# Kernel tuning notes

Measured on AMD Instinct MI355X. Metric: run time of the kernel, lower is better.

The kernel has to match this reference:

```python
import jax, jax.numpy as jnp
import numpy as np

B, S, D, H = 4, 2048, 1024, 16
HD = D // H
EPS = 1e-5
MASKED_BIAS = -10000.0

def setup_inputs() -> dict:
    key = jax.random.key(0)
    ks = jax.random.split(key, 12)
    sd = 0.02
    return {
        "hidden_states": jax.random.normal(ks[0], (B, S, D), jnp.float32),
        "Wq": jax.random.normal(ks[1], (D, D), jnp.float32) * sd,
        "bq": jnp.zeros((D,), jnp.float32),
        "Wk": jax.random.normal(ks[2], (D, D), jnp.float32) * sd,
        "bk": jnp.zeros((D,), jnp.float32),
        "Wv": jax.random.normal(ks[3], (D, D), jnp.float32) * sd,
        "bv": jnp.zeros((D,), jnp.float32),
        "Wp": jax.random.normal(ks[4], (D, D), jnp.float32) * sd,
        "bp": jnp.zeros((D,), jnp.float32),
        "ln_g": jnp.ones((D,), jnp.float32),
        "ln_b": jnp.zeros((D,), jnp.float32),
    }

def reference(hidden_states, Wq, bq, Wk, bk, Wv, bv, Wp, bp, ln_g, ln_b):
    x = hidden_states  # [B,S,D]
    # QKV projections (nn.Linear: x @ W^T + b; here W stored as [D,D], use x@W)
    q = x @ Wq + bq
    k = x @ Wk + bk
    v = x @ Wv + bv
    # split heads -> [B,H,S,HD]
    def split(t):
        return t.reshape(B, S, H, HD).transpose(0, 2, 1, 3)
    q, k, v = split(q), split(k), split(v)
    # scaled scores [B,H,S,S]
    scores = jnp.einsum("bhqd,bhkd->bhqk", q, k) / jnp.float32(np.sqrt(HD))
    causal = jnp.tril(jnp.ones((S, S), bool))
    scores = jnp.where(causal[None, None], scores, jnp.float32(MASKED_BIAS))
    attn = jax.nn.softmax(scores, axis=-1)
    out = jnp.einsum("bhqk,bhkd->bhqd", attn, v)
    # merge heads -> [B,S,D]
    out = out.transpose(0, 2, 1, 3).reshape(B, S, D)
    out = out @ Wp + bp
    # residual + layernorm
    y = out + x
    mu = jnp.mean(y, axis=-1, keepdims=True)
    var = jnp.var(y, axis=-1, keepdims=True)
    y = (y - mu) * jax.lax.rsqrt(var + EPS) * ln_g + ln_b
    return y
```

## Files before the change

kernel.cpp:

```cpp
#include <hip/hip_runtime.h>
#include <math.h>

#define B_  4
#define S_  2048
#define D_  1024
#define H_  16
#define HD_ 64
#define M_  (B_*S_)

typedef unsigned int  uint;
typedef unsigned short ushort;

typedef __attribute__((ext_vector_type(8))) short bf16x8;
typedef __attribute__((ext_vector_type(4))) float f32x4;

#if __has_builtin(__builtin_amdgcn_exp2f)
#define EXP2(x) __builtin_amdgcn_exp2f(x)
#else
#define EXP2(x) exp2f(x)
#endif

__device__ __forceinline__ ushort f2bf(float x) {
    uint u = __float_as_uint(x);
    u += 0x7FFFu + ((u >> 16) & 1u);
    return (ushort)(u >> 16);
}
__device__ __forceinline__ uint pack2bf(float a, float b) {
    uint ua = __float_as_uint(a); ua += 0x7FFFu + ((ua >> 16) & 1u);
    uint ub = __float_as_uint(b); ub += 0x7FFFu + ((ub >> 16) & 1u);
    return (ua >> 16) | (ub & 0xFFFF0000u);
}

__global__ __launch_bounds__(256) void prep(const float* __restrict__ x,
                                            ushort* __restrict__ xb,
                                            const float* __restrict__ Wq,
                                            const float* __restrict__ Wk,
                                            const float* __restrict__ Wv,
                                            const float* __restrict__ Wp,
                                            ushort* __restrict__ wtq,
                                            ushort* __restrict__ wtk,
                                            ushort* __restrict__ wtv,
                                            ushort* __restrict__ wtp) {
    __shared__ float t[32][33];
    const int tid = threadIdx.x;
    if (blockIdx.z == 0) {
        const int idx = blockIdx.x * 256 + tid;
        const float4* p = (const float4*)(x + (size_t)idx * 8);
        float4 a = p[0], b = p[1];
        uint4 o;
        o.x = pack2bf(a.x, a.y); o.y = pack2bf(a.z, a.w);
        o.z = pack2bf(b.x, b.y); o.w = pack2bf(b.z, b.w);
        ((uint4*)xb)[idx] = o;
    } else {
        const int w = blockIdx.x >> 10;
        const int sub = blockIdx.x & 1023;
        const float* W = (w == 0) ? Wq : (w == 1) ? Wk : (w == 2) ? Wv : Wp;
        ushort* Wt     = (w == 0) ? wtq : (w == 1) ? wtk : (w == 2) ? wtv : wtp;
        const int nb = (sub & 31) * 32, kb = (sub >> 5) * 32;
        #pragma unroll
        for (int l = 0; l < 4; ++l) {
            int idx = tid + l * 256;
            int r = idx >> 5, c = idx & 31;
            t[r][c] = W[(size_t)(kb + r) * D_ + nb + c];
        }
        __syncthreads();
        #pragma unroll
        for (int l = 0; l < 4; ++l) {
            int idx = tid + l * 256;
            int nr = idx >> 5, kc = idx & 31;
            Wt[(size_t)(nb + nr) * D_ + kb + kc] = f2bf(t[kc][nr]);
        }
    }
}

#define GM 128
#define GN 128
#define GK 32

__device__ __forceinline__ void gemm_core(const ushort* __restrict__ A,
                                          const ushort* __restrict__ Bt,
                                          f32x4 acc[4][4], int m0, int n0) {
    __shared__ __align__(16) ushort As[GM * GK];
    __shared__ __align__(16) ushort Bs[GN * GK];
    const int tid  = threadIdx.x;
    const int wave = tid >> 6, lane = tid & 63;
    const int wm = (wave >> 1) * 64, wn = (wave & 1) * 64;
    const int fr = lane & 15, fq = lane >> 4;

    #pragma unroll
    for (int i = 0; i < 4; ++i)
        #pragma unroll
        for (int j = 0; j < 4; ++j) acc[i][j] = (f32x4){0.f, 0.f, 0.f, 0.f};

    for (int k0 = 0; k0 < D_; k0 += GK) {
        #pragma unroll
        for (int it = 0; it < 2; ++it) {
            int ch = it * 256 + tid;
            int r = ch >> 2, p = ch & 3;
            const ushort* ga = A  + (size_t)(m0 + r) * D_ + k0 + p * 8;
            const ushort* gb = Bt + (size_t)(n0 + r) * D_ + k0 + p * 8;
            ushort* la = As + (size_t)(it * 256 + wave * 64) * 8;
            ushort* lb = Bs + (size_t)(it * 256 + wave * 64) * 8;
            __builtin_amdgcn_global_load_lds(
                (const __attribute__((address_space(1))) void*)ga,
                (__attribute__((address_space(3))) void*)la, 16, 0, 0);
            __builtin_amdgcn_global_load_lds(
                (const __attribute__((address_space(1))) void*)gb,
                (__attribute__((address_space(3))) void*)lb, 16, 0, 0);
        }
        __syncthreads();

        bf16x8 af[4], bfr[4];
        #pragma unroll
        for (int i = 0; i < 4; ++i)
            af[i] = *(const bf16x8*)&As[(wm + 16 * i + fr) * GK + fq * 8];
        #pragma unroll
        for (int j = 0; j < 4; ++j)
            bfr[j] = *(const bf16x8*)&Bs[(wn + 16 * j + fr) * GK + fq * 8];
        #pragma unroll
        for (int i = 0; i < 4; ++i)
            #pragma unroll
            for (int j = 0; j < 4; ++j)
                acc[i][j] = __builtin_amdgcn_mfma_f32_16x16x32_bf16(af[i], bfr[j], acc[i][j], 0, 0, 0);
        __syncthreads();
    }
}

__global__ __launch_bounds__(256) void gemm_qkvt(const ushort* __restrict__ xb,
                                                 const ushort* __restrict__ wtq,
                                                 const ushort* __restrict__ wtk,
                                                 const ushort* __restrict__ wtv,
                                                 const float* __restrict__ bq,
                                                 const float* __restrict__ bk,
                                                 const float* __restrict__ bv,
                                                 ushort* __restrict__ qb,
                                                 ushort* __restrict__ kb,
                                                 ushort* __restrict__ vtb) {
    const int z = blockIdx.z;
    const int lane = threadIdx.x & 63, wave = threadIdx.x >> 6;
    const int wm = (wave >> 1) * 64, wn = (wave & 1) * 64;
    const int cr = (lane >> 4) * 4, cc = lane & 15;
    f32x4 acc[4][4];

    if (z < 2) {
        const int m0 = blockIdx.x * GM, n0 = blockIdx.y * GN;
        gemm_core(xb, z ? wtk : wtq, acc, m0, n0);
        const float* bias = z ? bk : bq;
        ushort* C = z ? kb : qb;
        const float sc = z ? 1.0f : 0.18033688f;
        #pragma unroll
        for (int j = 0; j < 4; ++j) {
            const int col = n0 + wn + 16 * j + cc;
            const float bs = bias[col];
            const int h = col >> 6, hd = col & 63;
            #pragma unroll
            for (int i = 0; i < 4; ++i)
                #pragma unroll
                for (int r = 0; r < 4; ++r) {
                    const int row = m0 + wm + 16 * i + cr + r;
                    const int bb = row >> 11, s = row & 2047;
                    C[(((size_t)bb * H_ + h) * S_ + s) * HD_ + hd] = f2bf((acc[i][j][r] + bs) * sc);
                }
        }
    } else {
        const int m0 = blockIdx.y * GM, n0 = blockIdx.x * GN;
        gemm_core(wtv, xb, acc, m0, n0);
        #pragma unroll
        for (int i = 0; i < 4; ++i)
            #pragma unroll
            for (int r = 0; r < 4; ++r) {
                const int f = m0 + wm + 16 * i + cr + r;
                const float bs = bv[f];
                const int h = f >> 6, hd = f & 63;
                #pragma unroll
                for (int j = 0; j < 4; ++j) {
                    const int t = n0 + wn + 16 * j + cc;
                    const int bb = t >> 11, s = t & 2047;
                    vtb[(((size_t)bb * H_ + h) * HD_ + hd) * S_ + s] = f2bf(acc[i][j][r] + bs);
                }
            }
    }
}

__global__ __launch_bounds__(256) void gemm_p(const ushort* __restrict__ A,
                                              const ushort* __restrict__ Bt,
                                              const float* __restrict__ bias,
                                              float* __restrict__ C) {
    const int m0 = blockIdx.y * GM, n0 = blockIdx.x * GN;
    f32x4 acc[4][4];
    gemm_core(A, Bt, acc, m0, n0);

    const int lane = threadIdx.x & 63, wave = threadIdx.x >> 6;
    const int wm = (wave >> 1) * 64, wn = (wave & 1) * 64;
    const int cr = (lane >> 4) * 4, cc = lane & 15;
    #pragma unroll
    for (int j = 0; j < 4; ++j) {
        const int col = n0 + wn + 16 * j + cc;
        const float bs = bias[col];
        #pragma unroll
        for (int i = 0; i < 4; ++i)
            #pragma unroll
            for (int r = 0; r < 4; ++r)
                C[(size_t)(m0 + wm + 16 * i + cr + r) * D_ + col] = acc[i][j][r] + bs;
    }
}

#define PST 40

__global__ __launch_bounds__(256) void attn_mfma(const ushort* __restrict__ qb,
                                                 const ushort* __restrict__ kb,
                                                 const ushort* __restrict__ vtb,
                                                 ushort* __restrict__ ob) {
    __shared__ __align__(16) ushort Ks[2][128 * 64];
    __shared__ __align__(16) ushort Vs[2][64 * 128];
    __shared__ __align__(16) ushort Pp[4][32 * PST];

    const int tid = threadIdx.x, wave = tid >> 6, lane = tid & 63;
    const int fr = lane & 15, fq = lane >> 4;
    const int hb = blockIdx.x;
    const int p  = blockIdx.y;
    const int b = hb >> 4, h = hb & 15;
    const size_t bh = (size_t)b * H_ + h;
    const ushort* qbase = qb + bh * S_ * HD_;
    const ushort* kbase = kb + bh * S_ * HD_;
    const ushort* vbase = vtb + bh * HD_ * S_;
    ushort* PpW = Pp[wave];
    const int xrw = (fr & 7) << 4;

    int kg[4], vg[4];
    #pragma unroll
    for (int i = 0; i < 4; ++i) {
        const int o = (i * 256 + tid) * 16;
        int r = o >> 7, cS = o & 127;
        kg[i] = r * 128 + (cS ^ ((r & 7) << 4));
        r = o >> 8; cS = o & 255;
        vg[i] = r * (S_ * 2) + (cS ^ ((r & 7) << 4));
    }

    for (int phase = 0; phase < 2; ++phase) {
        const int chunk = phase ? p : (15 - p);
        const int q0 = chunk * 128;
        const int wq0 = q0 + wave * 32;
        const int nkt = chunk + 1;

        bf16x8 qf[2][2];
        #pragma unroll
        for (int nt = 0; nt < 2; ++nt)
            #pragma unroll
            for (int kk = 0; kk < 2; ++kk)
                qf[nt][kk] = *(const bf16x8*)&qbase[(size_t)(wq0 + nt * 16 + fr) * HD_ + kk * 32 + fq * 8];

        f32x4 ot[4][2];
        #pragma unroll
        for (int mt = 0; mt < 4; ++mt)
            #pragma unroll
            for (int nt = 0; nt < 2; ++nt) ot[mt][nt] = (f32x4){0.f, 0.f, 0.f, 0.f};
        float lp[2] = {0.f, 0.f};

        int cur = 0;
        #pragma unroll
        for (int i = 0; i < 4; ++i) {
            __builtin_amdgcn_global_load_lds(
                (const __attribute__((address_space(1))) void*)((const char*)kbase + kg[i]),
                (__attribute__((address_space(3))) void*)(&Ks[0][(i * 256 + wave * 64) * 8]), 16, 0, 0);
            __builtin_amdgcn_global_load_lds(
                (const __attribute__((address_space(1))) void*)((const char*)vbase + vg[i]),
                (__attribute__((address_space(3))) void*)(&Vs[0][(i * 256 + wave * 64) * 8]), 16, 0, 0);
        }
        __syncthreads();

        for (int kt = 0; kt < nkt; ++kt) {
            if (kt + 1 < nkt) {
                const int kn = (kt + 1) * 128;
                #pragma unroll
                for (int i = 0; i < 4; ++i) {
                    __builtin_amdgcn_global_load_lds(
                        (const __attribute__((address_space(1))) void*)((const char*)kbase + (size_t)kn * 128 + kg[i]),
                        (__attribute__((address_space(3))) void*)(&Ks[cur ^ 1][(i * 256 + wave * 64) * 8]), 16, 0, 0);
                    __builtin_amdgcn_global_load_lds(
                        (const __attribute__((address_space(1))) void*)((const char*)vbase + (size_t)kn * 2 + vg[i]),
                        (__attribute__((address_space(3))) void*)(&Vs[cur ^ 1][(i * 256 + wave * 64) * 8]), 16, 0, 0);
                }
            }
            const int k0 = kt * 128;
            const ushort* Kb = Ks[cur];
            const ushort* Vb = Vs[cur];
            const bool last = (kt == nkt - 1);

            #pragma unroll
            for (int g = 0; g < 4; ++g) {
                bf16x8 kf[2][2];
                #pragma unroll
                for (int mtL = 0; mtL < 2; ++mtL) {
                    const int mt = 2 * g + mtL;
                    kf[mtL][0] = *(const bf16x8*)((const char*)Kb + (mt * 16 + fr) * 128 + ((fq * 16) ^ xrw));
                    kf[mtL][1] = *(const bf16x8*)((const char*)Kb + (mt * 16 + fr) * 128 + ((64 + fq * 16) ^ xrw));
                }
                f32x4 st[2][2];
                #pragma unroll
                for (int mtL = 0; mtL < 2; ++mtL) {
                    const int mt = 2 * g + mtL;
                    #pragma unroll
                    for (int nt = 0; nt < 2; ++nt) {
                        f32x4 t = (f32x4){0.f, 0.f, 0.f, 0.f};
                        if (k0 + mt * 16 <= wq0 + nt * 16 + 15) {
                            t = __builtin_amdgcn_mfma_f32_16x16x32_bf16(kf[mtL][0], qf[nt][0], t, 0, 0, 0);
                            t = __builtin_amdgcn_mfma_f32_16x16x32_bf16(kf[mtL][1], qf[nt][1], t, 0, 0, 0);
                        }
                        st[mtL][nt] = t;
                    }
                }
                #pragma unroll
                for (int nt = 0; nt < 2; ++nt) {
                    const int qrow = wq0 + nt * 16 + fr;
                    #pragma unroll
                    for (int mtL = 0; mtL < 2; ++mtL) {
                        const int kb0 = k0 + (2 * g + mtL) * 16 + fq * 4;
                        float pr[4];
                        #pragma unroll
                        for (int r = 0; r < 4; ++r) {
                            const float e = EXP2(st[mtL][nt][r]);
                            pr[r] = (last && (kb0 + r > qrow)) ? 0.f : e;
                        }
                        lp[nt] += (pr[0] + pr[1]) + (pr[2] + pr[3]);
                        uint2 w;
                        w.x = pack2bf(pr[0], pr[1]);
                        w.y = pack2bf(pr[2], pr[3]);
                        *(uint2*)&PpW[(nt * 16 + fr) * PST + mtL * 16 + fq * 4] = w;
                    }
                }
                bf16x8 vf[4];
                #pragma unroll
                for (int mt = 0; mt < 4; ++mt)
                    vf[mt] = *(const bf16x8*)((const char*)Vb + (mt * 16 + fr) * 256 + ((g * 64 + fq * 16) ^ xrw));
                #pragma unroll
                for (int nt = 0; nt < 2; ++nt) {
                    if (k0 + g * 32 <= wq0 + nt * 16 + 15) {
                        bf16x8 pf = *(const bf16x8*)&PpW[(nt * 16 + fr) * PST + fq * 8];
                        #pragma unroll
                        for (int mt = 0; mt < 4; ++mt)
                            ot[mt][nt] = __builtin_amdgcn_mfma_f32_16x16x32_bf16(vf[mt], pf, ot[mt][nt], 0, 0, 0);
                    }
                }
            }
            __syncthreads();
            cur ^= 1;
        }

        #pragma unroll
        for (int nt = 0; nt < 2; ++nt) {
            float l = lp[nt];
            l += __shfl_xor(l, 16);
            l += __shfl_xor(l, 32);
            const float inv = 1.0f / l;
            const int row = wq0 + nt * 16 + fr;
            #pragma unroll
            for (int mt = 0; mt < 4; ++mt) {
                uint2 w;
                w.x = pack2bf(ot[mt][nt][0] * inv, ot[mt][nt][1] * inv);
                w.y = pack2bf(ot[mt][nt][2] * inv, ot[mt][nt][3] * inv);
                *(uint2*)&ob[((size_t)b * S_ + row) * D_ + h * HD_ + mt * 16 + fq * 4] = w;
            }
        }
    }
}

__global__ __launch_bounds__(256) void resln(float* __restrict__ out,
                                             const float* __restrict__ x,
                                             const float* __restrict__ g,
                                             const float* __restrict__ bb) {
    __shared__ float red[256];
    const int row = blockIdx.x, tid = threadIdx.x;
    const size_t off = (size_t)row * D_ + tid * 4;

    float4 p  = *(const float4*)&out[off];
    float4 xr = *(const float4*)&x[off];
    float4 y  = make_float4(p.x + xr.x, p.y + xr.y, p.z + xr.z, p.w + xr.w);

    float sum = y.x + y.y + y.z + y.w;
    red[tid] = sum;
    __syncthreads();
    #pragma unroll
    for (int st = 128; st > 0; st >>= 1) {
        if (tid < st) red[tid] += red[tid + st];
        __syncthreads();
    }
    const float mu = red[0] * (1.0f / D_);
    __syncthreads();

    float dx = y.x - mu, dy = y.y - mu, dz = y.z - mu, dw = y.w - mu;
    red[tid] = dx * dx + dy * dy + dz * dz + dw * dw;
    __syncthreads();
    #pragma unroll
    for (int st = 128; st > 0; st >>= 1) {
        if (tid < st) red[tid] += red[tid + st];
        __syncthreads();
    }
    const float var = red[0] * (1.0f / D_);
    const float inv = rsqrtf(var + 1e-5f);

    float4 gg = *(const float4*)&g[tid * 4];
    float4 bv = *(const float4*)&bb[tid * 4];
    float4 r;
    r.x = dx * inv * gg.x + bv.x;
    r.y = dy * inv * gg.y + bv.y;
    r.z = dz * inv * gg.z + bv.z;
    r.w = dw * inv * gg.w + bv.w;
    *(float4*)&out[off] = r;
}

extern "C" void kernel_launch(void* const* d_in, const int* in_sizes, int n_in,
                              void* d_out, int out_size, void* d_ws, size_t ws_size,
                              hipStream_t stream) {
    const float* x    = (const float*)d_in[0];
    const float* Wq   = (const float*)d_in[1];
    const float* bq   = (const float*)d_in[2];
    const float* Wk   = (const float*)d_in[3];
    const float* bk   = (const float*)d_in[4];
    const float* Wv   = (const float*)d_in[5];
    const float* bv   = (const float*)d_in[6];
    const float* Wp   = (const float*)d_in[7];
    const float* bp   = (const float*)d_in[8];
    const float* ln_g = (const float*)d_in[9];
    const float* ln_b = (const float*)d_in[10];

    float* out = (float*)d_out;

    char* ws = (char*)d_ws;
    ushort* qb  = (ushort*)ws;
    ushort* kb  = (ushort*)(ws + (size_t)16 * (1 << 20));
    ushort* vtb = (ushort*)(ws + (size_t)32 * (1 << 20));
    ushort* xb  = (ushort*)(ws + (size_t)48 * (1 << 20));
    ushort* ob  = (ushort*)(ws + (size_t)64 * (1 << 20));
    ushort* wtq = (ushort*)(ws + (size_t)80 * (1 << 20));
    ushort* wtk = (ushort*)(ws + (size_t)82 * (1 << 20));
    ushort* wtv = (ushort*)(ws + (size_t)84 * (1 << 20));
    ushort* wtp = (ushort*)(ws + (size_t)86 * (1 << 20));

    prep<<<dim3(4096, 1, 2), 256, 0, stream>>>(x, xb, Wq, Wk, Wv, Wp, wtq, wtk, wtv, wtp);

    gemm_qkvt<<<dim3(M_ / GM, D_ / GN, 3), 256, 0, stream>>>(
        xb, wtq, wtk, wtv, bq, bk, bv, qb, kb, vtb);

    attn_mfma<<<dim3(64, 8, 1), 256, 0, stream>>>(qb, kb, vtb, ob);

    gemm_p<<<dim3(D_ / GN, M_ / GM), 256, 0, stream>>>(ob, wtp, bp, out);
    resln<<<M_, 256, 0, stream>>>(out, x, ln_g, ln_b);
}
```

Measured before the change: 292.0 us.

## Peel causal tail tile, software-pipeline QK MFMAs, vectorize QKV epilogue stores

The attention loop now peels the last (diagonal) key tile so full tiles run without masking checks. In those tiles the QK^T MFMAs for the next group are issued before the exp and PV work of the current group, with s_setprio raised around MFMA bursts to overlap matrix and VALU work. The QKV GEMM swaps its MFMA operand order so each lane holds 4 contiguous output features (or tokens for V^T) and writes packed 8-byte stores instead of scalar bf16 stores. This adds register pressure from the double-buffered score fragments.

New measurement: 282.2 us. -3.4%, faster.

```diff
diff --git a/kernel.cpp b/kernel.cpp
--- a/kernel.cpp
+++ b/kernel.cpp
@@ -77,6 +77,7 @@
 #define GN 128
 #define GK 32
 
+template <bool SWAP>
 __device__ __forceinline__ void gemm_core(const ushort* __restrict__ A,
                                           const ushort* __restrict__ Bt,
                                           f32x4 acc[4][4], int m0, int n0) {
@@ -121,7 +122,9 @@
         for (int i = 0; i < 4; ++i)
             #pragma unroll
             for (int j = 0; j < 4; ++j)
-                acc[i][j] = __builtin_amdgcn_mfma_f32_16x16x32_bf16(af[i], bfr[j], acc[i][j], 0, 0, 0);
+                acc[i][j] = SWAP
+                    ? __builtin_amdgcn_mfma_f32_16x16x32_bf16(bfr[j], af[i], acc[i][j], 0, 0, 0)
+                    : __builtin_amdgcn_mfma_f32_16x16x32_bf16(af[i], bfr[j], acc[i][j], 0, 0, 0);
         __syncthreads();
     }
 }
@@ -139,46 +142,49 @@
     const int z = blockIdx.z;
     const int lane = threadIdx.x & 63, wave = threadIdx.x >> 6;
     const int wm = (wave >> 1) * 64, wn = (wave & 1) * 64;
-    const int cr = (lane >> 4) * 4, cc = lane & 15;
+    const int cc = lane & 15, fq = lane >> 4;
+    const int m0 = blockIdx.x * GM, n0 = blockIdx.y * GN;
     f32x4 acc[4][4];
 
     if (z < 2) {
-        const int m0 = blockIdx.x * GM, n0 = blockIdx.y * GN;
-        gemm_core(xb, z ? wtk : wtq, acc, m0, n0);
+        gemm_core<true>(xb, z ? wtk : wtq, acc, m0, n0);
         const float* bias = z ? bk : bq;
         ushort* C = z ? kb : qb;
         const float sc = z ? 1.0f : 0.18033688f;
         #pragma unroll
         for (int j = 0; j < 4; ++j) {
-            const int col = n0 + wn + 16 * j + cc;
-            const float bs = bias[col];
-            const int h = col >> 6, hd = col & 63;
-            #pragma unroll
-            for (int i = 0; i < 4; ++i)
-                #pragma unroll
-                for (int r = 0; r < 4; ++r) {
-                    const int row = m0 + wm + 16 * i + cr + r;
-                    const int bb = row >> 11, s = row & 2047;
-                    C[(((size_t)bb * H_ + h) * S_ + s) * HD_ + hd] = f2bf((acc[i][j][r] + bs) * sc);
-                }
+            const int f0 = n0 + wn + 16 * j + fq * 4;
+            const float4 bs4 = *(const float4*)&bias[f0];
+            const int h = f0 >> 6, hd = f0 & 63;
+            #pragma unroll
+            for (int i = 0; i < 4; ++i) {
+                const int token = m0 + wm + 16 * i + cc;
+                const int bb = token >> 11, s = token & 2047;
+                const float v0 = (acc[i][j][0] + bs4.x) * sc;
+                const float v1 = (acc[i][j][1] + bs4.y) * sc;
+                const float v2 = (acc[i][j][2] + bs4.z) * sc;
+                const float v3 = (acc[i][j][3] + bs4.w) * sc;
+                uint2 w; w.x = pack2bf(v0, v1); w.y = pack2bf(v2, v3);
+                *(uint2*)&C[(((size_t)bb * H_ + h) * S_ + s) * HD_ + hd] = w;
+            }
         }
     } else {
-        const int m0 = blockIdx.y * GM, n0 = blockIdx.x * GN;
-        gemm_core(wtv, xb, acc, m0, n0);
-        #pragma unroll
-        for (int i = 0; i < 4; ++i)
-            #pragma unroll
-            for (int r = 0; r < 4; ++r) {
-                const int f = m0 + wm + 16 * i + cr + r;
+        gemm_core<false>(xb, wtv, acc, m0, n0);
+        #pragma unroll
+        for (int i = 0; i < 4; ++i) {
+            const int t0 = m0 + wm + 16 * i + fq * 4;
+            const int bb = t0 >> 11, s = t0 & 2047;
+            #pragma unroll
+            for (int j = 0; j < 4; ++j) {
+                const int f = n0 + wn + 16 * j + cc;
                 const float bs = bv[f];
                 const int h = f >> 6, hd = f & 63;
-                #pragma unroll
-                for (int j = 0; j < 4; ++j) {
-                    const int t = n0 + wn + 16 * j + cc;
-                    const int bb = t >> 11, s = t & 2047;
-                    vtb[(((size_t)bb * H_ + h) * HD_ + hd) * S_ + s] = f2bf(acc[i][j][r] + bs);
-                }
+                uint2 w;
+                w.x = pack2bf(acc[i][j][0] + bs, acc[i][j][1] + bs);
+                w.y = pack2bf(acc[i][j][2] + bs, acc[i][j][3] + bs);
+                *(uint2*)&vtb[(((size_t)bb * H_ + h) * HD_ + hd) * S_ + s] = w;
             }
+        }
     }
 }
 
@@ -188,7 +194,7 @@
                                               float* __restrict__ C) {
     const int m0 = blockIdx.y * GM, n0 = blockIdx.x * GN;
     f32x4 acc[4][4];
-    gemm_core(A, Bt, acc, m0, n0);
+    gemm_core<false>(A, Bt, acc, m0, n0);
 
     const int lane = threadIdx.x & 63, wave = threadIdx.x >> 6;
     const int wm = (wave >> 1) * 64, wn = (wave & 1) * 64;
@@ -206,6 +212,18 @@
 }
 
 #define PST 40
+
+#define STAGE(kt_, buf_) do {                                                   \
+    const int kn_ = (kt_) * 128;                                                \
+    _Pragma("unroll")                                                           \
+    for (int i_ = 0; i_ < 4; ++i_) {                                            \
+        __builtin_amdgcn_global_load_lds(                                       \
+            (const __attribute__((address_space(1))) void*)((const char*)kbase + (size_t)kn_ * 128 + kg[i_]), \
+            (__attribute__((address_space(3))) void*)(&Ks[buf_][(i_ * 256 + wave * 64) * 8]), 16, 0, 0); \
+        __builtin_amdgcn_global_load_lds(                                       \
+            (const __attribute__((address_space(1))) void*)((const char*)vbase + (size_t)kn_ * 2 + vg[i_]), \
+            (__attribute__((address_space(3))) void*)(&Vs[buf_][(i_ * 256 + wave * 64) * 8]), 16, 0, 0); \
+    } } while (0)
 
 __global__ __launch_bounds__(256) void attn_mfma(const ushort* __restrict__ qb,
                                                  const ushort* __restrict__ kb,
@@ -258,34 +276,92 @@
         float lp[2] = {0.f, 0.f};
 
         int cur = 0;
-        #pragma unroll
-        for (int i = 0; i < 4; ++i) {
-            __builtin_amdgcn_global_load_lds(
-                (const __attribute__((address_space(1))) void*)((const char*)kbase + kg[i]),
-                (__attribute__((address_space(3))) void*)(&Ks[0][(i * 256 + wave * 64) * 8]), 16, 0, 0);
-            __builtin_amdgcn_global_load_lds(
-                (const __attribute__((address_space(1))) void*)((const char*)vbase + vg[i]),
-                (__attribute__((address_space(3))) void*)(&Vs[0][(i * 256 + wave * 64) * 8]), 16, 0, 0);
-        }
+        STAGE(0, 0);
         __syncthreads();
 
-        for (int kt = 0; kt < nkt; ++kt) {
-            if (kt + 1 < nkt) {
-                const int kn = (kt + 1) * 128;
-                #pragma unroll
-                for (int i = 0; i < 4; ++i) {
-                    __builtin_amdgcn_global_load_lds(
-                        (const __attribute__((address_space(1))) void*)((const char*)kbase + (size_t)kn * 128 + kg[i]),
-                        (__attribute__((address_space(3))) void*)(&Ks[cur ^ 1][(i * 256 + wave * 64) * 8]), 16, 0, 0);
-                    __builtin_amdgcn_global_load_lds(
-                        (const __attribute__((address_space(1))) void*)((const char*)vbase + (size_t)kn * 2 + vg[i]),
-                        (__attribute__((address_space(3))) void*)(&Vs[cur ^ 1][(i * 256 + wave * 64) * 8]), 16, 0, 0);
-                }
-            }
-            const int k0 = kt * 128;
+        for (int kt = 0; kt < nkt - 1; ++kt) {
+            STAGE(kt + 1, cur ^ 1);
             const ushort* Kb = Ks[cur];
             const ushort* Vb = Vs[cur];
-            const bool last = (kt == nkt - 1);
+
+            bf16x8 kf[2][2][2];
+            f32x4  st[2][2][2];
+
+            #pragma unroll
+            for (int mtL = 0; mtL < 2; ++mtL) {
+                kf[0][mtL][0] = *(const bf16x8*)((const char*)Kb + (mtL * 16 + fr) * 128 + ((fq * 16) ^ xrw));
+                kf[0][mtL][1] = *(const bf16x8*)((const char*)Kb + (mtL * 16 + fr) * 128 + ((64 + fq * 16) ^ xrw));
+            }
+            __builtin_amdgcn_s_setprio(1);
+            #pragma unroll
+            for (int mtL = 0; mtL < 2; ++mtL)
+                #pragma unroll
+                for (int nt = 0; nt < 2; ++nt) {
+                    f32x4 t = (f32x4){0.f, 0.f, 0.f, 0.f};
+                    t = __builtin_amdgcn_mfma_f32_16x16x32_bf16(kf[0][mtL][0], qf[nt][0], t, 0, 0, 0);
+                    t = __builtin_amdgcn_mfma_f32_16x16x32_bf16(kf[0][mtL][1], qf[nt][1], t, 0, 0, 0);
+                    st[0][mtL][nt] = t;
+                }
+            __builtin_amdgcn_s_setprio(0);
+
+            #pragma unroll
+            for (int g = 0; g < 4; ++g) {
+                const int pc = g & 1, pn = pc ^ 1;
+                if (g < 3) {
+                    const int mtb = 2 * (g + 1);
+                    #pragma unroll
+                    for (int mtL = 0; mtL < 2; ++mtL) {
+                        kf[pn][mtL][0] = *(const bf16x8*)((const char*)Kb + ((mtb + mtL) * 16 + fr) * 128 + ((fq * 16) ^ xrw));
+                        kf[pn][mtL][1] = *(const bf16x8*)((const char*)Kb + ((mtb + mtL) * 16 + fr) * 128 + ((64 + fq * 16) ^ xrw));
+                    }
+                    __builtin_amdgcn_s_setprio(1);
+                    #pragma unroll
+                    for (int mtL = 0; mtL < 2; ++mtL)
+                        #pragma unroll
+                        for (int nt = 0; nt < 2; ++nt) {
+                            f32x4 t = (f32x4){0.f, 0.f, 0.f, 0.f};
+                            t = __builtin_amdgcn_mfma_f32_16x16x32_bf16(kf[pn][mtL][0], qf[nt][0], t, 0, 0, 0);
+                            t = __builtin_amdgcn_mfma_f32_16x16x32_bf16(kf[pn][mtL][1], qf[nt][1], t, 0, 0, 0);
+                            st[pn][mtL][nt] = t;
+                        }
+                    __builtin_amdgcn_s_setprio(0);
+                }
+                #pragma unroll
+                for (int nt = 0; nt < 2; ++nt) {
+                    #pragma unroll
+                    for (int mtL = 0; mtL < 2; ++mtL) {
+                        float pr[4];
+                        #pragma unroll
+                        for (int r = 0; r < 4; ++r) pr[r] = EXP2(st[pc][mtL][nt][r]);
+                        uint2 w;
+                        w.x = pack2bf(pr[0], pr[1]);
+                        w.y = pack2bf(pr[2], pr[3]);
+                        *(uint2*)&PpW[(nt * 16 + fr) * PST + mtL * 16 + fq * 4] = w;
+                        lp[nt] += (pr[0] + pr[1]) + (pr[2] + pr[3]);
+                    }
+                }
+                bf16x8 vf[4];
+                #pragma unroll
+                for (int mt = 0; mt < 4; ++mt)
+                    vf[mt] = *(const bf16x8*)((const char*)Vb + (mt * 16 + fr) * 256 + ((g * 64 + fq * 16) ^ xrw));
+                #pragma unroll
+                for (int nt = 0; nt < 2; ++nt) {
+                    bf16x8 pf = *(const bf16x8*)&PpW[(nt * 16 + fr) * PST + fq * 8];
+                    __builtin_amdgcn_s_setprio(1);
+                    #pragma unroll
+                    for (int mt = 0; mt < 4; ++mt)
+                        ot[mt][nt] = __builtin_amdgcn_mfma_f32_16x16x32_bf16(vf[mt], pf, ot[mt][nt], 0, 0, 0);
+                    __builtin_amdgcn_s_setprio(0);
+                }
+            }
+            __syncthreads();
+            cur ^= 1;
+        }
+
+        {
+            const int k0 = (nkt - 1) * 128;
+            const ushort* Kb = Ks[cur];
+            const ushort* Vb = Vs[cur];
 
             #pragma unroll
             for (int g = 0; g < 4; ++g) {
@@ -304,8 +380,10 @@
                     for (int nt = 0; nt < 2; ++nt) {
                         f32x4 t = (f32x4){0.f, 0.f, 0.f, 0.f};
                         if (k0 + mt * 16 <= wq0 + nt * 16 + 15) {
+                            __builtin_amdgcn_s_setprio(1);
                             t = __builtin_amdgcn_mfma_f32_16x16x32_bf16(kf[mtL][0], qf[nt][0], t, 0, 0, 0);
                             t = __builtin_amdgcn_mfma_f32_16x16x32_bf16(kf[mtL][1], qf[nt][1], t, 0, 0, 0);
+                            __builtin_amdgcn_s_setprio(0);
                         }
                         st[mtL][nt] = t;
                     }
@@ -320,7 +398,7 @@
                         #pragma unroll
                         for (int r = 0; r < 4; ++r) {
                             const float e = EXP2(st[mtL][nt][r]);
-                            pr[r] = (last && (kb0 + r > qrow)) ? 0.f : e;
+                            pr[r] = (kb0 + r > qrow) ? 0.f : e;
                         }
                         lp[nt] += (pr[0] + pr[1]) + (pr[2] + pr[3]);
                         uint2 w;
@@ -337,14 +415,15 @@
                 for (int nt = 0; nt < 2; ++nt) {
                     if (k0 + g * 32 <= wq0 + nt * 16 + 15) {
                         bf16x8 pf = *(const bf16x8*)&PpW[(nt * 16 + fr) * PST + fq * 8];
+                        __builtin_amdgcn_s_setprio(1);
                         #pragma unroll
                         for (int mt = 0; mt < 4; ++mt)
                             ot[mt][nt] = __builtin_amdgcn_mfma_f32_16x16x32_bf16(vf[mt], pf, ot[mt][nt], 0, 0, 0);
+                        __builtin_amdgcn_s_setprio(0);
                     }
                 }
             }
             __syncthreads();
-            cur ^= 1;
         }
 
         #pragma unroll
```
